# Kernel optimization log

Measured on AMD Instinct MI355X. Metric: run time of the kernel, lower is better.

Reference implementation:

```python
import jax, jax.numpy as jnp
import numpy as np

B, I, H = 65536, 512, 128
T, ES, EC = 2, 2, 4  # tasks, specific experts per task, common experts
ETOT = ES + EC


def setup_inputs() -> dict:
    key = jax.random.key(0)
    ks = jax.random.split(key, 9)
    s = 0.02
    return {
        "x": jax.random.normal(ks[0], (B, I), dtype=jnp.float32),
        "Wc": jax.random.normal(ks[1], (EC, I, H), dtype=jnp.float32) * s,
        "bc": jax.random.normal(ks[2], (EC, H), dtype=jnp.float32) * s,
        "Ws": jax.random.normal(ks[3], (T, ES, I, H), dtype=jnp.float32) * s,
        "bs": jax.random.normal(ks[4], (T, ES, H), dtype=jnp.float32) * s,
        "Wg": jax.random.normal(ks[5], (T, ETOT * H, ETOT), dtype=jnp.float32) * s,
        "bg": jax.random.normal(ks[6], (T, ETOT), dtype=jnp.float32) * s,
        "Wt": jax.random.normal(ks[7], (T, H, 1), dtype=jnp.float32) * s,
        "bt": jax.random.normal(ks[8], (T, 1), dtype=jnp.float32) * s,
    }


def reference(x, Wc, bc, Ws, bs, Wg, bg, Wt, bt):
    # Common experts: [EC, B, H]
    common = jnp.einsum("bi,eih->ebh", x, Wc) + bc[:, None, :]
    # Task-specific experts: [T, ES, B, H]
    spec = jnp.einsum("bi,teih->tebh", x, Ws) + bs[:, :, None, :]
    # Per task: experts ordered [specific..., common...] -> [T, ETOT, B, H]
    tmp = jnp.concatenate(
        [spec, jnp.broadcast_to(common[None], (T,) + common.shape)], axis=1
    )
    # Gate input: per-sample concat of all expert outputs -> [T, B, ETOT*H]
    gate_in = tmp.transpose(0, 2, 1, 3).reshape(T, B, ETOT * H)
    weights = jax.nn.softmax(
        jnp.einsum("tbf,tfe->tbe", gate_in, Wg) + bg[:, None, :], axis=-1
    )  # [T, B, ETOT]
    feature = jnp.einsum("tbe,tebh->tbh", weights, tmp)  # [T, B, H]
    out = jnp.einsum("tbh,tho->tbo", feature, Wt) + bt[:, None, :]  # [T, B, 1]
    return out
```

## Files before the change

### kernel.cpp

```cpp
#include <hip/hip_runtime.h>
#include <math.h>

#define BB 65536
#define II 512
#define HH 128
#define TT 2
#define ES 2
#define EC 4
#define NS 6
#define NJ 12
#define NCOL 24
#define NCOLP 32
#define FF (NS * HH)
#define KSTEPS (II / 32)

typedef _Float16 f16;
typedef f16   half8 __attribute__((ext_vector_type(8)));
typedef float f32x4 __attribute__((ext_vector_type(4)));


#define FFP (FF + 4)

__global__ __launch_bounds__(256) void cgc_precompute(
    const float* __restrict__ Wc, const float* __restrict__ bc,
    const float* __restrict__ Ws, const float* __restrict__ bs,
    const float* __restrict__ Wg, const float* __restrict__ bg,
    const float* __restrict__ Wt,
    f16* __restrict__ Mfrag, float* __restrict__ d)
{
    __shared__ float wrow[TT * FF];
    __shared__ float wgt[TT * NS * FFP];
    __shared__ float wt[TT * HH];
    __shared__ float red[NCOL][9];

    const int blk = blockIdx.x;
    const bool isd = (blk == II);
    const int i   = blk;
    const int tid = threadIdx.x;

    {
        const float4* Wg4 = (const float4*)Wg;
        for (int idx = tid; idx < TT * FF * NS / 4; idx += 256) {
            const float4 v = Wg4[idx];
            const int p0 = idx * 4;
            const float vv[4] = {v.x, v.y, v.z, v.w};
            #pragma unroll
            for (int u = 0; u < 4; ++u) {
                const int p = p0 + u;
                const int t = p / (FF * NS);
                const int r = p % (FF * NS);
                const int f = r / NS;
                const int e = r % NS;
                wgt[(t * NS + e) * FFP + f] = vv[u];
            }
        }
        if (tid < TT * HH / 4)
            ((float4*)wt)[tid] = ((const float4*)Wt)[tid];
    }
    {
        const float4* Ws4 = (const float4*)Ws;
        const float4* Wc4 = (const float4*)Wc;
        const float4* bs4 = (const float4*)bs;
        const float4* bc4 = (const float4*)bc;
        float4* wr4 = (float4*)wrow;
        for (int idx = tid; idx < TT * FF / 4; idx += 256) {
            const int t   = idx / (FF / 4);
            const int rem = idx % (FF / 4);
            const int s   = rem >> 5;
            const int h4  = rem & 31;
            float4 v;
            if (isd) {
                v = (s < ES) ? bs4[(t * ES + s) * 32 + h4]
                             : bc4[(s - ES) * 32 + h4];
            } else {
                v = (s < ES) ? Ws4[((t * ES + s) * II + i) * 32 + h4]
                             : Wc4[((s - ES) * II + i) * 32 + h4];
            }
            wr4[idx] = v;
        }
    }
    __syncthreads();

    const int col = tid >> 3;
    const int fp  = tid & 7;
    if (col < NCOL) {
        const int t = col / NJ;
        const int j = col % NJ;
        float acc = 0.0f;
        if (j < NS) {
            const float* wr  = &wrow[t * FF];
            const float* wgr = &wgt[(t * NS + j) * FFP];
            #pragma unroll 4
            for (int ff = 0; ff < FF / 8; ++ff) {
                const int f = ff * 8 + fp;
                acc = fmaf(wr[f], wgr[f], acc);
            }
        } else {
            const int s = j - NS;
            const float* wr  = &wrow[t * FF + s * HH];
            const float* wtr = &wt[t * HH];
            #pragma unroll
            for (int hh = 0; hh < HH / 8; ++hh) {
                const int h = hh * 8 + fp;
                acc = fmaf(wr[h], wtr[h], acc);
            }
        }
        red[col][fp] = acc;
    }
    __syncthreads();

    if (tid < NCOLP) {
        float v = 0.0f;
        if (tid < NCOL) {
            #pragma unroll
            for (int p = 0; p < 8; ++p) v += red[tid][p];
        }
        if (isd) {
            if (tid < NCOL) {
                const int t = tid / NJ, j = tid % NJ;
                if (j < NS) v += bg[t * NS + j];
                d[tid] = v;
            }
        } else {
            const int step = i >> 5;
            const int kk   = i & 31;
            const int g    = (kk >> 2) & 3;
            const int s    = ((kk >> 4) << 2) | (kk & 3);
            const int ct   = tid >> 4;
            const int ln   = g * 16 + (tid & 15);
            Mfrag[((((step * 2 + ct) * 64) + ln) << 3) + s] = (f16)v;
        }
    }
}

#define RT 2
#define ZP 25

union Sh2 {
    uint4 bfrag[KSTEPS * 2 * 64];
    float zbuf[128][ZP];
};

__device__ __forceinline__ half8 uint4_as_half8(uint4 u) {
    union { uint4 u; half8 h; } c; c.u = u; return c.h;
}

__global__ __launch_bounds__(256, 2) void cgc_main(
    const float* __restrict__ x,
    const f16* __restrict__ Mfrag,
    const float* __restrict__ dg,
    const float* __restrict__ bt,
    float* __restrict__ out)
{
    __shared__ Sh2 sh;

    const int tid  = threadIdx.x;
    const int wv   = tid >> 6;
    const int lane = tid & 63;
    const int cl   = lane & 15;
    const int g    = lane >> 4;
    const int r0   = blockIdx.x * 128;

    {
        const uint4* Mf4 = (const uint4*)Mfrag;
        #pragma unroll
        for (int it = 0; it < (KSTEPS * 2 * 64) / 256; ++it)
            sh.bfrag[it * 256 + tid] = Mf4[it * 256 + tid];
    }
    __syncthreads();

    f32x4 acc[RT][2];
    #pragma unroll
    for (int rt = 0; rt < RT; ++rt)
        #pragma unroll
        for (int ct = 0; ct < 2; ++ct)
            acc[rt][ct] = (f32x4){0.f, 0.f, 0.f, 0.f};

    const float* xp0 = x + (size_t)(r0 + wv * 32 + cl) * II + g * 4;
    const float* xp1 = xp0 + 16 * II;

    #pragma unroll 4
    for (int s = 0; s < KSTEPS; ++s) {
        const uint4* bp = &sh.bfrag[s * 128 + lane];
        const half8 b0 = uint4_as_half8(bp[0]);
        const half8 b1 = uint4_as_half8(bp[64]);
        #pragma unroll
        for (int rt = 0; rt < RT; ++rt) {
            const float* xp = (rt == 0 ? xp0 : xp1) + s * 32;
            const f32x4 xa = *(const f32x4*)(xp);
            const f32x4 xb = *(const f32x4*)(xp + 16);
            half8 a;
            a[0] = (f16)xa[0]; a[1] = (f16)xa[1];
            a[2] = (f16)xa[2]; a[3] = (f16)xa[3];
            a[4] = (f16)xb[0]; a[5] = (f16)xb[1];
            a[6] = (f16)xb[2]; a[7] = (f16)xb[3];
            acc[rt][0] = __builtin_amdgcn_mfma_f32_16x16x32_f16(a, b0, acc[rt][0], 0, 0, 0);
            acc[rt][1] = __builtin_amdgcn_mfma_f32_16x16x32_f16(a, b1, acc[rt][1], 0, 0, 0);
        }
    }

    const float dv0 = dg[cl];
    const float dv1 = (cl < 8) ? dg[16 + cl] : 0.f;

    __syncthreads();

    #pragma unroll
    for (int rt = 0; rt < RT; ++rt) {
        const int rr = wv * 32 + rt * 16 + g * 4;
        #pragma unroll
        for (int q = 0; q < 4; ++q) {
            sh.zbuf[rr + q][cl] = acc[rt][0][q] + dv0;
            if (cl < 8)
                sh.zbuf[rr + q][16 + cl] = acc[rt][1][q] + dv1;
        }
    }
    __syncthreads();

    {
        const int row = tid & 127;
        const int t   = tid >> 7;
        const float* zr = &sh.zbuf[row][t * NJ];
        float m = zr[0];
        #pragma unroll
        for (int j = 1; j < NS; ++j) m = fmaxf(m, zr[j]);
        float ssum = 0.f, o = 0.f;
        #pragma unroll
        for (int j = 0; j < NS; ++j) {
            const float e = __expf(zr[j] - m);
            ssum += e;
            o += e * zr[NS + j];
        }
        out[t * BB + r0 + row] = o / ssum + bt[t];
    }
}

extern "C" void kernel_launch(void* const* d_in, const int* in_sizes, int n_in,
                              void* d_out, int out_size, void* d_ws, size_t ws_size,
                              hipStream_t stream)
{
    const float* x  = (const float*)d_in[0];
    const float* Wc = (const float*)d_in[1];
    const float* bc = (const float*)d_in[2];
    const float* Ws = (const float*)d_in[3];
    const float* bs = (const float*)d_in[4];
    const float* Wg = (const float*)d_in[5];
    const float* bg = (const float*)d_in[6];
    const float* Wt = (const float*)d_in[7];
    const float* bt = (const float*)d_in[8];
    float* out = (float*)d_out;

    f16*   Mfrag = (f16*)d_ws;
    float* d     = (float*)((char*)d_ws + KSTEPS * 2 * 64 * 16);

    cgc_precompute<<<dim3(II + 1), dim3(256), 0, stream>>>(
        Wc, bc, Ws, bs, Wg, bg, Wt, Mfrag, d);
    cgc_main<<<dim3(BB / 128), dim3(256), 0, stream>>>(
        x, Mfrag, d, bt, out);
}
```

Before: 214.5 us.

## Halve rows per block, raise occupancy, and prefetch next x tile in registers

Each block now covers 64 rows instead of 128, so each wave computes a single 16-row MFMA tile, and the launch bound moves from 2 to 4 blocks per CU. The K loop is fully unrolled and software-pipelined: the next step's x values are loaded into registers while the current step is converted and multiplied. The goal is to hide global-load latency on x, the dominant HBM stream, through more resident waves and explicit prefetch. In exchange, twice as many blocks each reload the 32KB B fragment into LDS, and each wave has less independent MFMA work per step.

Result: no change. 213.6 us (-0.4%).

```diff
diff --git a/kernel.cpp b/kernel.cpp
--- a/kernel.cpp
+++ b/kernel.cpp
@@ -133,19 +133,19 @@
     }
 }
 
-#define RT 2
+#define ROWSB 64
 #define ZP 25
 
 union Sh2 {
     uint4 bfrag[KSTEPS * 2 * 64];
-    float zbuf[128][ZP];
+    float zbuf[ROWSB][ZP];
 };
 
 __device__ __forceinline__ half8 uint4_as_half8(uint4 u) {
     union { uint4 u; half8 h; } c; c.u = u; return c.h;
 }
 
-__global__ __launch_bounds__(256, 2) void cgc_main(
+__global__ __launch_bounds__(256, 4) void cgc_main(
     const float* __restrict__ x,
     const f16* __restrict__ Mfrag,
     const float* __restrict__ dg,
@@ -159,7 +159,7 @@
     const int lane = tid & 63;
     const int cl   = lane & 15;
     const int g    = lane >> 4;
-    const int r0   = blockIdx.x * 128;
+    const int r0   = blockIdx.x * ROWSB;
 
     {
         const uint4* Mf4 = (const uint4*)Mfrag;
@@ -169,34 +169,32 @@
     }
     __syncthreads();
 
-    f32x4 acc[RT][2];
+    f32x4 acc0 = (f32x4){0.f, 0.f, 0.f, 0.f};
+    f32x4 acc1 = (f32x4){0.f, 0.f, 0.f, 0.f};
+
+    const float* xp = x + (size_t)(r0 + wv * 16 + cl) * II + g * 4;
+
+    f32x4 xa = *(const f32x4*)(xp);
+    f32x4 xb = *(const f32x4*)(xp + 16);
+
     #pragma unroll
-    for (int rt = 0; rt < RT; ++rt)
-        #pragma unroll
-        for (int ct = 0; ct < 2; ++ct)
-            acc[rt][ct] = (f32x4){0.f, 0.f, 0.f, 0.f};
-
-    const float* xp0 = x + (size_t)(r0 + wv * 32 + cl) * II + g * 4;
-    const float* xp1 = xp0 + 16 * II;
-
-    #pragma unroll 4
     for (int s = 0; s < KSTEPS; ++s) {
+        f32x4 na, nb;
+        if (s + 1 < KSTEPS) {
+            na = *(const f32x4*)(xp + (s + 1) * 32);
+            nb = *(const f32x4*)(xp + (s + 1) * 32 + 16);
+        }
         const uint4* bp = &sh.bfrag[s * 128 + lane];
         const half8 b0 = uint4_as_half8(bp[0]);
         const half8 b1 = uint4_as_half8(bp[64]);
-        #pragma unroll
-        for (int rt = 0; rt < RT; ++rt) {
-            const float* xp = (rt == 0 ? xp0 : xp1) + s * 32;
-            const f32x4 xa = *(const f32x4*)(xp);
-            const f32x4 xb = *(const f32x4*)(xp + 16);
-            half8 a;
-            a[0] = (f16)xa[0]; a[1] = (f16)xa[1];
-            a[2] = (f16)xa[2]; a[3] = (f16)xa[3];
-            a[4] = (f16)xb[0]; a[5] = (f16)xb[1];
-            a[6] = (f16)xb[2]; a[7] = (f16)xb[3];
-            acc[rt][0] = __builtin_amdgcn_mfma_f32_16x16x32_f16(a, b0, acc[rt][0], 0, 0, 0);
-            acc[rt][1] = __builtin_amdgcn_mfma_f32_16x16x32_f16(a, b1, acc[rt][1], 0, 0, 0);
-        }
+        half8 a;
+        a[0] = (f16)xa[0]; a[1] = (f16)xa[1];
+        a[2] = (f16)xa[2]; a[3] = (f16)xa[3];
+        a[4] = (f16)xb[0]; a[5] = (f16)xb[1];
+        a[6] = (f16)xb[2]; a[7] = (f16)xb[3];
+        acc0 = __builtin_amdgcn_mfma_f32_16x16x32_f16(a, b0, acc0, 0, 0, 0);
+        acc1 = __builtin_amdgcn_mfma_f32_16x16x32_f16(a, b1, acc1, 0, 0, 0);
+        xa = na; xb = nb;
     }
 
     const float dv0 = dg[cl];
@@ -204,21 +202,20 @@
 
     __syncthreads();
 
-    #pragma unroll
-    for (int rt = 0; rt < RT; ++rt) {
-        const int rr = wv * 32 + rt * 16 + g * 4;
+    {
+        const int rr = wv * 16 + g * 4;
         #pragma unroll
         for (int q = 0; q < 4; ++q) {
-            sh.zbuf[rr + q][cl] = acc[rt][0][q] + dv0;
+            sh.zbuf[rr + q][cl] = acc0[q] + dv0;
             if (cl < 8)
-                sh.zbuf[rr + q][16 + cl] = acc[rt][1][q] + dv1;
-        }
-    }
-    __syncthreads();
-
-    {
-        const int row = tid & 127;
-        const int t   = tid >> 7;
+                sh.zbuf[rr + q][16 + cl] = acc1[q] + dv1;
+        }
+    }
+    __syncthreads();
+
+    if (tid < ROWSB * TT) {
+        const int row = tid & (ROWSB - 1);
+        const int t   = tid >> 6;
         const float* zr = &sh.zbuf[row][t * NJ];
         float m = zr[0];
         #pragma unroll
@@ -254,6 +251,6 @@
 
     cgc_precompute<<<dim3(II + 1), dim3(256), 0, stream>>>(
         Wc, bc, Ws, bs, Wg, bg, Wt, Mfrag, d);
-    cgc_main<<<dim3(BB / 128), dim3(256), 0, stream>>>(
+    cgc_main<<<dim3(BB / ROWSB), dim3(256), 0, stream>>>(
         x, Mfrag, d, bt, out);
 }
```
